# Kernel optimization log

Measured on AMD Instinct MI355X. Metric: run time of the kernel, lower is better.

Reference implementation:

```python
import jax, jax.numpy as jnp
import numpy as np

EMBED = 768
HIDDEN = 768
HEADS = 12
HEAD_DIM = HIDDEN // HEADS


def setup_inputs() -> dict:
    key = jax.random.key(0)
    ks = jax.random.split(key, 9)
    B, S = 16, 512
    lim = 1.0 / np.sqrt(EMBED)
    def lin(kw, kb):
        W = jax.random.uniform(kw, (EMBED, HIDDEN), jnp.float32, -lim, lim)
        b = jax.random.uniform(kb, (HIDDEN,), jnp.float32, -lim, lim)
        return W, b
    Wq, bq = lin(ks[0], ks[1])
    Wk, bk = lin(ks[2], ks[3])
    Wv, bv = lin(ks[4], ks[5])
    inp = jax.random.normal(ks[6], (B, S, EMBED), jnp.float32)
    mask = jax.random.randint(ks[7], (B, S), 0, 2).astype(jnp.float32)
    return {"input": inp, "input_mask": mask,
            "Wq": Wq, "bq": bq, "Wk": Wk, "bk": bk, "Wv": Wv, "bv": bv}


def reference(input, input_mask, Wq, bq, Wk, bk, Wv, bv):
    B, S, _ = input.shape
    # projections -> (B, H, S, D)
    def proj(W, b):
        x = jnp.einsum('bse,eh->bsh', input, W) + b
        return x.reshape(B, S, HEADS, HEAD_DIM).transpose(0, 2, 1, 3)
    Q = proj(Wq, bq)
    K = proj(Wk, bk)
    V = proj(Wv, bv)
    # scores (B, H, S, S), additive mask over keys
    scores = jnp.einsum('bhqd,bhkd->bhqk', Q, K) / jnp.sqrt(jnp.float32(HEAD_DIM))
    bias = (input_mask * -1e9)[:, None, None, :]  # (B,1,1,S) broadcast over heads & queries
    weight = jax.nn.softmax(scores + bias, axis=-1)
    out = jnp.einsum('bhqk,bhkd->bhqd', weight, V)
    return out.transpose(0, 2, 1, 3).reshape(B, S, HIDDEN)
```

## Files before the change

### kernel.cpp

```cpp
#include <hip/hip_runtime.h>
#include <hip/hip_bf16.h>
#include <cstdint>
#include <cstddef>

#define B_  16
#define S_  512
#define E_  768
#define NH_ 12
#define D_  64
#define M_  (B_*S_)

typedef unsigned short u16;
typedef __attribute__((ext_vector_type(4))) float f32x4;
typedef __attribute__((ext_vector_type(8))) short bf16x8;

#define LOG2E 1.4426950408889634f

__device__ __forceinline__ u16 f2bf(float f){
  union { float fv; uint32_t u; } v; v.fv = f;
  uint32_t u = v.u;
  uint32_t r = u + 0x7fffu + ((u >> 16) & 1u);
  return (u16)(r >> 16);
}

__device__ __forceinline__ void gload_lds16(const u16* g, u16* l){
  __builtin_amdgcn_global_load_lds(
      (const __attribute__((address_space(1))) void*)g,
      (__attribute__((address_space(3))) void*)l, 16, 0, 0);
}

__global__ __launch_bounds__(256) void prep_kernel(
    const float* __restrict__ X, u16* __restrict__ Xb,
    const float* __restrict__ Wq, const float* __restrict__ Wk,
    const float* __restrict__ Wv, u16* __restrict__ WtBase)
{
  __shared__ float t[32][33];
  const int bx = blockIdx.x;
  if (bx < 6144){
    int i = bx * 256 + threadIdx.x;
    float4 v = reinterpret_cast<const float4*>(X)[i];
    ushort4 o;
    o.x = f2bf(v.x); o.y = f2bf(v.y); o.z = f2bf(v.z); o.w = f2bf(v.w);
    reinterpret_cast<ushort4*>(Xb)[i] = o;
  } else {
    int tt = bx - 6144;
    int z = tt / 576, rem = tt % 576;
    int byi = rem / 24, bxi = rem % 24;
    const float* W = (z == 0) ? Wq : ((z == 1) ? Wk : Wv);
    u16* Wt = WtBase + (size_t)z * E_ * E_;
    int bx0 = bxi * 32, by0 = byi * 32;
    int tx = threadIdx.x & 31, ty = threadIdx.x >> 5;
    #pragma unroll
    for (int i = 0; i < 32; i += 8)
      t[ty + i][tx] = W[(size_t)(by0 + ty + i) * E_ + bx0 + tx];
    __syncthreads();
    #pragma unroll
    for (int i = 0; i < 32; i += 8)
      Wt[(size_t)(bx0 + ty + i) * E_ + by0 + tx] = f2bf(t[tx][ty + i]);
  }
}

__global__ __launch_bounds__(256) void qkv_gemm_kernel(
    const u16* __restrict__ Xb, const u16* __restrict__ WtBase,
    const float* __restrict__ bq, const float* __restrict__ bk, const float* __restrict__ bv,
    u16* __restrict__ Qb, u16* __restrict__ Kb, u16* __restrict__ VtB)
{
  __shared__ u16 lA[2][16 * 512];
  __shared__ u16 lB[2][16 * 512];
  const int z = blockIdx.z;
  const u16* Wt = WtBase + (size_t)z * E_ * E_;
  const float* bias = (z == 0) ? bq : ((z == 1) ? bk : bv);
  const int m0 = blockIdx.x * 128;
  const int n0 = blockIdx.y * 128;
  const int tid = threadIdx.x;
  const int lane = tid & 63;
  const int wave = tid >> 6;
  const int wm = wave & 1, wn = wave >> 1;
  const int col0 = lane & 15, quad = lane >> 4;
  const int rslot = quad*16 + (col0 ^ (quad << 1));
  const int oct_l = lane >> 4;
  const int row_l = (lane & 15) ^ (oct_l << 1);

  f32x4 acc[4][4];
  #pragma unroll
  for (int i = 0; i < 4; ++i)
    #pragma unroll
    for (int j = 0; j < 4; ++j)
      acc[i][j] = (f32x4){0.f, 0.f, 0.f, 0.f};

  const u16* gA = Xb + (size_t)(m0 + wave*16 + row_l) * E_ + oct_l*8;
  const u16* gB = Wt + (size_t)(n0 + wave*16 + row_l) * E_ + oct_l*8;

  auto stage = [&](int k0, int buf){
    #pragma unroll
    for (int i = 0; i < 4; ++i){
      int rh = i >> 1, kh = i & 1;
      int c = (rh*4 + wave)*2 + kh;
      gload_lds16(gA + (size_t)rh*64*E_ + k0 + kh*32, &lA[buf][c*512]);
      gload_lds16(gB + (size_t)rh*64*E_ + k0 + kh*32, &lB[buf][c*512]);
    }
  };
  stage(0, 0);

  #pragma unroll 1
  for (int st = 0; st < 12; ++st){
    const int cur = st & 1;
    __syncthreads();
    if (st < 11) stage((st + 1) * 64, cur ^ 1);
    const u16* la = &lA[cur][0];
    const u16* lb = &lB[cur][0];
    #pragma unroll
    for (int ks = 0; ks < 2; ++ks){
      bf16x8 af[4], bfr[4];
      #pragma unroll
      for (int mi = 0; mi < 4; ++mi)
        af[mi] = *reinterpret_cast<const bf16x8*>(&la[((wm*4 + mi)*2 + ks)*512 + rslot*8]);
      #pragma unroll
      for (int ni = 0; ni < 4; ++ni)
        bfr[ni] = *reinterpret_cast<const bf16x8*>(&lb[((wn*4 + ni)*2 + ks)*512 + rslot*8]);
      #pragma unroll
      for (int mi = 0; mi < 4; ++mi)
        #pragma unroll
        for (int ni = 0; ni < 4; ++ni)
          acc[mi][ni] = __builtin_amdgcn_mfma_f32_16x16x32_bf16(af[mi], bfr[ni], acc[mi][ni], 0, 0, 0);
    }
  }

  #pragma unroll
  for (int mi = 0; mi < 4; ++mi){
    #pragma unroll
    for (int ni = 0; ni < 4; ++ni){
      int n = n0 + wn*64 + ni*16 + col0;
      float bval = bias[n];
      int h = n >> 6, d = n & 63;
      #pragma unroll
      for (int r = 0; r < 4; ++r){
        int m = m0 + wm*64 + mi*16 + quad*4 + r;
        int b = m >> 9, s = m & 511;
        u16 obf = f2bf(acc[mi][ni][r] + bval);
        size_t bh = (size_t)b * NH_ + h;
        if (z == 0)      Qb[(bh * S_ + s) * D_ + d] = obf;
        else if (z == 1) Kb[(bh * S_ + s) * D_ + d] = obf;
        else             VtB[(bh * D_ + d) * S_ + s] = obf;
      }
    }
  }
}

__global__ __launch_bounds__(256) void attn_kernel(
    const u16* __restrict__ Qb, const u16* __restrict__ Kb, const u16* __restrict__ VtB,
    const float* __restrict__ mask, float* __restrict__ out)
{
  __shared__ u16 lK[2][8 * 512];
  __shared__ u16 lV[2][8 * 512];
  __shared__ u16 lP[8 * 1024];
  __shared__ float biasS[S_];
  const int bh = blockIdx.x;
  const int qt = blockIdx.y;
  const int b = bh / NH_, h = bh % NH_;
  const int tid = threadIdx.x, lane = tid & 63, wave = tid >> 6;
  const int col0 = lane & 15, quad = lane >> 4;
  const int ls = lane & 15, lk = lane >> 4;
  const float C1 = 0.125f * LOG2E;

  for (int i = tid; i < S_; i += 256)
    biasS[i] = mask[b * S_ + i] * (-1.0e9f * LOG2E);

  const u16* Kbh = Kb  + (size_t)bh * S_ * D_;
  const u16* Vbh = VtB + (size_t)bh * D_ * S_;

  bf16x8 qf[2][2];
  #pragma unroll
  for (int g = 0; g < 2; ++g){
    int qrow = qt*128 + wave*32 + g*16 + col0;
    #pragma unroll
    for (int ks = 0; ks < 2; ++ks)
      qf[g][ks] = *reinterpret_cast<const bf16x8*>(
          Qb + ((size_t)bh * S_ + qrow) * D_ + ks*32 + quad*8);
  }

  uint4 rg[4];
  auto issue = [&](int st){
    if (wave < 2){
      #pragma unroll
      for (int gg = 0; gg < 4; ++gg){
        int c = wave*4 + gg, ks = c >> 2, nt = c & 3;
        rg[gg] = *reinterpret_cast<const uint4*>(
            Kbh + (size_t)(st*64 + nt*16 + ls) * D_ + ks*32 + lk*8);
      }
    } else {
      #pragma unroll
      for (int gg = 0; gg < 4; ++gg){
        int c = (wave - 2)*4 + gg, ks2 = c >> 2, nd = c & 3;
        rg[gg] = *reinterpret_cast<const uint4*>(
            Vbh + (size_t)(nd*16 + ls) * S_ + st*64 + ks2*32 + lk*8);
      }
    }
  };
  issue(0);

  f32x4 o[2][4];
  #pragma unroll
  for (int g = 0; g < 2; ++g)
    #pragma unroll
    for (int i = 0; i < 4; ++i) o[g][i] = (f32x4){0.f, 0.f, 0.f, 0.f};
  float psum[2] = {0.f, 0.f};

  #pragma unroll 1
  for (int st = 0; st < 8; ++st){
    const int cur = st & 1;
    if (wave < 2){
      #pragma unroll
      for (int gg = 0; gg < 4; ++gg)
        *reinterpret_cast<uint4*>(&lK[cur][(wave*4 + gg)*512 + lane*8]) = rg[gg];
    } else {
      #pragma unroll
      for (int gg = 0; gg < 4; ++gg)
        *reinterpret_cast<uint4*>(&lV[cur][((wave - 2)*4 + gg)*512 + lane*8]) = rg[gg];
    }
    __syncthreads();
    if (st < 7) issue(st + 1);

    f32x4 sc[2][4];
    #pragma unroll
    for (int g = 0; g < 2; ++g)
      #pragma unroll
      for (int nt = 0; nt < 4; ++nt) sc[g][nt] = (f32x4){0.f, 0.f, 0.f, 0.f};
    #pragma unroll
    for (int ks = 0; ks < 2; ++ks){
      bf16x8 kf[4];
      #pragma unroll
      for (int nt = 0; nt < 4; ++nt)
        kf[nt] = *reinterpret_cast<const bf16x8*>(&lK[cur][(ks*4 + nt)*512 + lane*8]);
      #pragma unroll
      for (int g = 0; g < 2; ++g)
        #pragma unroll
        for (int nt = 0; nt < 4; ++nt)
          sc[g][nt] = __builtin_amdgcn_mfma_f32_16x16x32_bf16(kf[nt], qf[g][ks], sc[g][nt], 0, 0, 0);
    }

    float4 bb[4];
    #pragma unroll
    for (int nt = 0; nt < 4; ++nt)
      bb[nt] = *reinterpret_cast<const float4*>(&biasS[st*64 + nt*16 + quad*4]);

    #pragma unroll
    for (int g = 0; g < 2; ++g){
      #pragma unroll
      for (int nt = 0; nt < 4; ++nt){
        float p0 = exp2f(sc[g][nt][0] * C1 + bb[nt].x);
        float p1 = exp2f(sc[g][nt][1] * C1 + bb[nt].y);
        float p2 = exp2f(sc[g][nt][2] * C1 + bb[nt].z);
        float p3 = exp2f(sc[g][nt][3] * C1 + bb[nt].w);
        psum[g] += (p0 + p1) + (p2 + p3);
        float2 ab; ab.x = p0; ab.y = p1;
        float2 cd; cd.x = p2; cd.y = p3;
        __hip_bfloat162 h01 = __float22bfloat162_rn(ab);
        __hip_bfloat162 h23 = __float22bfloat162_rn(cd);
        uint2 pw;
        pw.x = *reinterpret_cast<unsigned int*>(&h01);
        pw.y = *reinterpret_cast<unsigned int*>(&h23);
        int addr = (wave*2 + g)*1024 + (nt >> 1)*512
                 + (((nt & 1)*2 + (quad >> 1))*16 + col0)*8 + (quad & 1)*4;
        *reinterpret_cast<uint2*>(&lP[addr]) = pw;
      }
    }

    #pragma unroll
    for (int ks2 = 0; ks2 < 2; ++ks2){
      bf16x8 pf0 = *reinterpret_cast<const bf16x8*>(&lP[(wave*2 + 0)*1024 + ks2*512 + lane*8]);
      bf16x8 pf1 = *reinterpret_cast<const bf16x8*>(&lP[(wave*2 + 1)*1024 + ks2*512 + lane*8]);
      #pragma unroll
      for (int nd = 0; nd < 4; ++nd){
        bf16x8 vf = *reinterpret_cast<const bf16x8*>(&lV[cur][(ks2*4 + nd)*512 + lane*8]);
        o[0][nd] = __builtin_amdgcn_mfma_f32_16x16x32_bf16(pf0, vf, o[0][nd], 0, 0, 0);
        o[1][nd] = __builtin_amdgcn_mfma_f32_16x16x32_bf16(pf1, vf, o[1][nd], 0, 0, 0);
      }
    }
  }

  #pragma unroll
  for (int g = 0; g < 2; ++g){
    float tot = psum[g];
    tot += __shfl_xor(tot, 16, 64);
    tot += __shfl_xor(tot, 32, 64);
    #pragma unroll
    for (int r = 0; r < 4; ++r){
      int s = qt*128 + wave*32 + g*16 + quad*4 + r;
      float lr = __shfl(tot, (lane & 48) | (quad*4 + r), 64);
      float inv = 1.0f / lr;
      #pragma unroll
      for (int nd = 0; nd < 4; ++nd){
        int d = nd*16 + col0;
        out[((size_t)b * S_ + s) * E_ + h*D_ + d] = o[g][nd][r] * inv;
      }
    }
  }
}

extern "C" void kernel_launch(void* const* d_in, const int* in_sizes, int n_in,
                              void* d_out, int out_size, void* d_ws, size_t ws_size,
                              hipStream_t stream){
  const float* X    = (const float*)d_in[0];
  const float* mask = (const float*)d_in[1];
  const float* Wq   = (const float*)d_in[2];
  const float* bq   = (const float*)d_in[3];
  const float* Wk   = (const float*)d_in[4];
  const float* bk   = (const float*)d_in[5];
  const float* Wv   = (const float*)d_in[6];
  const float* bv   = (const float*)d_in[7];
  float* out = (float*)d_out;

  u16* Xb = (u16*)d_ws;
  u16* Wt = Xb + (size_t)M_ * E_;
  u16* Qb = Wt + (size_t)3 * E_ * E_;
  u16* Kb = Qb + (size_t)M_ * E_;
  u16* Vt = Kb + (size_t)M_ * E_;

  prep_kernel<<<6144 + 1728, 256, 0, stream>>>(X, Xb, Wq, Wk, Wv, Wt);
  qkv_gemm_kernel<<<dim3(64, 6, 3), 256, 0, stream>>>(Xb, Wt, bq, bk, bv, Qb, Kb, Vt);
  attn_kernel<<<dim3(192, 4), 256, 0, stream>>>(Qb, Kb, Vt, mask, out);
}
```

Before: 216.8 us.

## Enlarge QKV GEMM tile to 128x256 with 8 waves and triple-buffered LDS

The QKV projection GEMM now runs 512 threads per block over a 128x256 output tile instead of 256 threads over 128x128. It replaces the static double-buffered LDS with a dynamic triple-buffered ring of 144KB. The K loop prefetches two stages ahead and waits with an explicit vmcnt so one stage of global-to-LDS loads stays in flight during compute. This is meant to hide load latency and raise reuse of the A tile, at the cost of one block per CU and fewer blocks (576) in the grid.

Measured after the change: 210.8 us. -2.8%, faster.

```diff
diff --git a/kernel.cpp b/kernel.cpp
--- a/kernel.cpp
+++ b/kernel.cpp
@@ -60,18 +60,20 @@
   }
 }
 
-__global__ __launch_bounds__(256) void qkv_gemm_kernel(
+__global__ __launch_bounds__(512) void qkv_gemm_kernel(
     const u16* __restrict__ Xb, const u16* __restrict__ WtBase,
     const float* __restrict__ bq, const float* __restrict__ bk, const float* __restrict__ bv,
     u16* __restrict__ Qb, u16* __restrict__ Kb, u16* __restrict__ VtB)
 {
-  __shared__ u16 lA[2][16 * 512];
-  __shared__ u16 lB[2][16 * 512];
+  extern __shared__ u16 lds[];
+  u16* ldsA = lds;
+  u16* ldsB = lds + 3 * 8192;
+
   const int z = blockIdx.z;
   const u16* Wt = WtBase + (size_t)z * E_ * E_;
   const float* bias = (z == 0) ? bq : ((z == 1) ? bk : bv);
   const int m0 = blockIdx.x * 128;
-  const int n0 = blockIdx.y * 128;
+  const int n0 = blockIdx.y * 256;
   const int tid = threadIdx.x;
   const int lane = tid & 63;
   const int wave = tid >> 6;
@@ -88,27 +90,24 @@
     for (int j = 0; j < 4; ++j)
       acc[i][j] = (f32x4){0.f, 0.f, 0.f, 0.f};
 
-  const u16* gA = Xb + (size_t)(m0 + wave*16 + row_l) * E_ + oct_l*8;
-  const u16* gB = Wt + (size_t)(n0 + wave*16 + row_l) * E_ + oct_l*8;
+  const u16* pA  = Xb + (size_t)(m0 + wave*16 + row_l) * E_ + oct_l*8;
+  const u16* pB0 = Wt + (size_t)(n0 + wave*32 + row_l) * E_ + oct_l*8;
+  const u16* pB1 = pB0 + (size_t)16 * E_;
 
   auto stage = [&](int k0, int buf){
-    #pragma unroll
-    for (int i = 0; i < 4; ++i){
-      int rh = i >> 1, kh = i & 1;
-      int c = (rh*4 + wave)*2 + kh;
-      gload_lds16(gA + (size_t)rh*64*E_ + k0 + kh*32, &lA[buf][c*512]);
-      gload_lds16(gB + (size_t)rh*64*E_ + k0 + kh*32, &lB[buf][c*512]);
-    }
+    u16* la = ldsA + buf * 8192;
+    u16* lb = ldsB + buf * 16384;
+    gload_lds16(pA  + k0,      la + (2*wave    )*512);
+    gload_lds16(pA  + k0 + 32, la + (2*wave + 1)*512);
+    gload_lds16(pB0 + k0,      lb + (4*wave    )*512);
+    gload_lds16(pB0 + k0 + 32, lb + (4*wave + 1)*512);
+    gload_lds16(pB1 + k0,      lb + (4*wave + 2)*512);
+    gload_lds16(pB1 + k0 + 32, lb + (4*wave + 3)*512);
   };
-  stage(0, 0);
-
-  #pragma unroll 1
-  for (int st = 0; st < 12; ++st){
-    const int cur = st & 1;
-    __syncthreads();
-    if (st < 11) stage((st + 1) * 64, cur ^ 1);
-    const u16* la = &lA[cur][0];
-    const u16* lb = &lB[cur][0];
+
+  auto compute = [&](int buf){
+    const u16* la = ldsA + buf * 8192;
+    const u16* lb = ldsB + buf * 16384;
     #pragma unroll
     for (int ks = 0; ks < 2; ++ks){
       bf16x8 af[4], bfr[4];
@@ -124,7 +123,23 @@
         for (int ni = 0; ni < 4; ++ni)
           acc[mi][ni] = __builtin_amdgcn_mfma_f32_16x16x32_bf16(af[mi], bfr[ni], acc[mi][ni], 0, 0, 0);
     }
-  }
+  };
+
+  stage(0, 0);
+  stage(64, 1);
+
+  #pragma unroll 1
+  for (int st = 0; st < 11; ++st){
+    asm volatile("s_waitcnt vmcnt(6)" ::: "memory");
+    __builtin_amdgcn_s_barrier();
+    __builtin_amdgcn_sched_barrier(0);
+    if (st < 10) stage((st + 2) * 64, (st + 2) % 3);
+    compute(st % 3);
+  }
+  asm volatile("s_waitcnt vmcnt(0)" ::: "memory");
+  __builtin_amdgcn_s_barrier();
+  __builtin_amdgcn_sched_barrier(0);
+  compute(2);
 
   #pragma unroll
   for (int mi = 0; mi < 4; ++mi){
@@ -318,6 +333,6 @@
   u16* Vt = Kb + (size_t)M_ * E_;
 
   prep_kernel<<<6144 + 1728, 256, 0, stream>>>(X, Xb, Wq, Wk, Wv, Wt);
-  qkv_gemm_kernel<<<dim3(64, 6, 3), 256, 0, stream>>>(Xb, Wt, bq, bk, bv, Qb, Kb, Vt);
+  qkv_gemm_kernel<<<dim3(64, 3, 3), 512, 147456, stream>>>(Xb, Wt, bq, bk, bv, Qb, Kb, Vt);
   attn_kernel<<<dim3(192, 4), 256, 0, stream>>>(Qb, Kb, Vt, mask, out);
 }
```
